# Kernel tuning notes

Measured on AMD Instinct MI355X. Metric: run time of the kernel, lower is better.

## Reference

```python
import jax, jax.numpy as jnp
import numpy as np

HEAD_COUNT = 8  # matches init_kwargs head_count

def _branch(q_in, k_in, v_in, Wq, bq, Wk, bk, Wv, bv):
    # q_in/k_in/v_in: [B, N, D]. Linear (efficient) attention, per-head.
    B, N, D = q_in.shape
    H = HEAD_COUNT
    hd = D // H
    q = q_in @ Wq + bq            # [B, N, D]
    k = k_in @ Wk + bk
    v = v_in @ Wv + bv
    # permute(0,2,1) then contiguous channel slices per head == [B,H,hd,N]
    q = q.reshape(B, N, H, hd).transpose(0, 2, 3, 1)  # [B,H,hd,Nq]
    k = k.reshape(B, N, H, hd).transpose(0, 2, 3, 1)  # [B,H,hd,Nk]
    v = v.reshape(B, N, H, hd).transpose(0, 2, 3, 1)  # [B,H,hd,Nk]
    q = jax.nn.softmax(q, axis=3)  # softmax over sequence positions (torch dim=2)
    k = jax.nn.softmax(k, axis=2)  # softmax over head channels (torch dim=1)
    # context = k @ v^T : [B,H,hd_c,hd_d]
    ctx = jnp.einsum('bhcn,bhdn->bhcd', k, v)
    # attended = context^T @ q : [B,H,hd_d,Nq]
    att = jnp.einsum('bhcd,bhcn->bhdn', ctx, q)
    # concat heads along channel dim, then transpose -> [B, Nq, D]
    return att.reshape(B, D, N).transpose(0, 2, 1)

def setup_inputs() -> dict:
    key = jax.random.key(0)
    ks = jax.random.split(key, 16)
    B, N, D = 4, 8192, 256
    s = 0.02
    inp = {
        'f1': jax.random.normal(ks[0], (B, N, D), jnp.float32),
        'f2': jax.random.normal(ks[1], (B, N, D), jnp.float32),
        'f3': jax.random.normal(ks[2], (B, N, D), jnp.float32),
        'f4': jax.random.normal(ks[3], (B, N, D), jnp.float32),
        'f1_pos_embed': jax.random.normal(ks[4], (B, N, D), jnp.float32),
        'f2_pos_embed': jax.random.normal(ks[5], (B, N, D), jnp.float32),
        'f3_pos_embed': jax.random.normal(ks[6], (B, N, D), jnp.float32),
        'f4_pos_embed': jax.random.normal(ks[7], (B, N, D), jnp.float32),
        'Wq': jax.random.normal(ks[8], (3, D, D), jnp.float32) * s,
        'bq': jax.random.normal(ks[9], (3, D), jnp.float32) * s,
        'Wk': jax.random.normal(ks[10], (3, D, D), jnp.float32) * s,
        'bk': jax.random.normal(ks[11], (3, D), jnp.float32) * s,
        'Wv': jax.random.normal(ks[12], (3, D, D), jnp.float32) * s,
        'bv': jax.random.normal(ks[13], (3, D), jnp.float32) * s,
        'Wrp': jax.random.normal(ks[14], (3 * D, D), jnp.float32) * s,
        'brp': jax.random.normal(ks[15], (D,), jnp.float32) * s,
    }
    return inp

def reference(f1, f2, f3, f4, f1_pos_embed, f2_pos_embed, f3_pos_embed, f4_pos_embed,
              Wq, bq, Wk, bk, Wv, bv, Wrp, brp):
    q_in = f1 + f1_pos_embed
    agg21 = _branch(q_in, f2 + f2_pos_embed, f2, Wq[0], bq[0], Wk[0], bk[0], Wv[0], bv[0])
    agg31 = _branch(q_in, f3 + f3_pos_embed, f3, Wq[1], bq[1], Wk[1], bk[1], Wv[1], bv[1])
    agg41 = _branch(q_in, f4 + f4_pos_embed, f4, Wq[2], bq[2], Wk[2], bk[2], Wv[2], bv[2])
    out = jnp.concatenate([agg21, agg31, agg41], axis=-1)  # [B, N, 3D]
    return out @ Wrp + brp  # dropout p=0.0 -> identity
```

## Files before the change

kernel.cpp:

```cpp
#include <hip/hip_runtime.h>
#include <hip/hip_bf16.h>

typedef __attribute__((ext_vector_type(8))) short short8;
typedef __attribute__((ext_vector_type(4))) float floatx4;
typedef __attribute__((ext_vector_type(16))) float floatx16;

#define N_SEQ 8192
#define M_ROWS 32768

__device__ __forceinline__ unsigned short f2bf(float f) {
    unsigned int x = __builtin_bit_cast(unsigned int, f);
    x += 0x7fff + ((x >> 16) & 1);
    return (unsigned short)(x >> 16);
}

__global__ __launch_bounds__(256) void transpose_w(
    const float* __restrict__ Wq, const float* __restrict__ Wk,
    const float* __restrict__ Wv, unsigned short* __restrict__ Wt)
{
    int job = blockIdx.x;
    int k = blockIdx.y;
    int n = threadIdx.x;
    const float* src =
        (job < 3) ? (Wq + job * 65536) :
        (job < 6) ? (Wk + (job - 3) * 65536) :
                    (Wv + (job - 6) * 65536);
    Wt[(size_t)job * 65536 + n * 256 + k] = f2bf(src[k * 256 + n]);
}

__global__ __launch_bounds__(256) void projq_kernel(
    const float* __restrict__ f1, const float* __restrict__ p1,
    const float* __restrict__ bq, const unsigned short* __restrict__ Wt,
    unsigned short* __restrict__ expQ, float* __restrict__ S)
{
    __shared__ __align__(16) unsigned short As[64][264];
    int m0 = blockIdx.x * 64;
    int b = m0 >> 13;
    int tid = threadIdx.x;
    int lane = tid & 63, wave = tid >> 6;
    int wm = wave >> 1, wn = wave & 1;
    int quad = lane >> 4, l15 = lane & 15;

    {
        int row = tid >> 2, seg = tid & 3;
        const float* fr = f1 + (size_t)(m0 + row) * 256 + seg * 64;
        const float* pr = p1 + (size_t)(m0 + row) * 256 + seg * 64;
        #pragma unroll
        for (int q = 0; q < 8; q++) {
            float4 x0 = *(const float4*)(fr + q * 8);
            float4 x1 = *(const float4*)(fr + q * 8 + 4);
            float4 y0 = *(const float4*)(pr + q * 8);
            float4 y1 = *(const float4*)(pr + q * 8 + 4);
            short8 v;
            v[0] = (short)f2bf(x0.x + y0.x); v[1] = (short)f2bf(x0.y + y0.y);
            v[2] = (short)f2bf(x0.z + y0.z); v[3] = (short)f2bf(x0.w + y0.w);
            v[4] = (short)f2bf(x1.x + y1.x); v[5] = (short)f2bf(x1.y + y1.y);
            v[6] = (short)f2bf(x1.z + y1.z); v[7] = (short)f2bf(x1.w + y1.w);
            *(short8*)&As[row][seg * 64 + q * 8] = v;
        }
    }
    __syncthreads();

    for (int nj = 0; nj < 6; nj++) {
        int j = nj >> 1;
        int n0 = (nj & 1) * 128;
        const unsigned short* Wj = Wt + (size_t)j * 65536;

        floatx4 acc[2][4];
        #pragma unroll
        for (int sm = 0; sm < 2; sm++)
            #pragma unroll
            for (int sn = 0; sn < 4; sn++)
                #pragma unroll
                for (int r = 0; r < 4; r++) acc[sm][sn][r] = 0.0f;

        #pragma unroll
        for (int ks = 0; ks < 8; ks++) {
            short8 af[2], bfr[4];
            #pragma unroll
            for (int sm = 0; sm < 2; sm++)
                af[sm] = *(const short8*)&As[wm * 32 + sm * 16 + l15][ks * 32 + quad * 8];
            #pragma unroll
            for (int sn = 0; sn < 4; sn++) {
                int ncol = n0 + wn * 64 + sn * 16 + l15;
                bfr[sn] = *(const short8*)(Wj + (size_t)ncol * 256 + ks * 32 + quad * 8);
            }
            #pragma unroll
            for (int sm = 0; sm < 2; sm++)
                #pragma unroll
                for (int sn = 0; sn < 4; sn++)
                    acc[sm][sn] = __builtin_amdgcn_mfma_f32_16x16x32_bf16(
                        af[sm], bfr[sn], acc[sm][sn], 0, 0, 0);
        }

        float colsum[4] = {0.f, 0.f, 0.f, 0.f};
        #pragma unroll
        for (int sm = 0; sm < 2; sm++)
            #pragma unroll
            for (int sn = 0; sn < 4; sn++) {
                float bb = bq[j * 256 + n0 + wn * 64 + sn * 16 + l15];
                #pragma unroll
                for (int r = 0; r < 4; r++) {
                    float e = __expf(acc[sm][sn][r] + bb);
                    colsum[sn] += e;
                    int row = m0 + wm * 32 + sm * 16 + quad * 4 + r;
                    int col = j * 256 + n0 + wn * 64 + sn * 16 + l15;
                    expQ[(size_t)row * 768 + col] = f2bf(e);
                }
            }
        #pragma unroll
        for (int sn = 0; sn < 4; sn++) {
            float v = colsum[sn];
            v += __shfl_xor(v, 16, 64);
            v += __shfl_xor(v, 32, 64);
            if (quad == 0)
                atomicAdd(&S[b * 768 + j * 256 + n0 + wn * 64 + sn * 16 + l15], v);
        }
    }
}

__global__ __launch_bounds__(256) void projkv_ctx(
    const float* __restrict__ f2, const float* __restrict__ f3, const float* __restrict__ f4,
    const float* __restrict__ p2, const float* __restrict__ p3, const float* __restrict__ p4,
    const float* __restrict__ bk, const float* __restrict__ bv,
    const unsigned short* __restrict__ Wt, float* __restrict__ ctx)
{
    __shared__ __align__(16) unsigned short Ak[64][264];
    __shared__ __align__(16) unsigned short Av[64][264];

    int blk = blockIdx.x;
    int c = blk & 31;
    int ib = blk >> 5;
    int b = ib & 3, i = ib >> 2;
    const float* fin = ((i == 0) ? f2 : (i == 1) ? f3 : f4) + (size_t)b * N_SEQ * 256;
    const float* pin = ((i == 0) ? p2 : (i == 1) ? p3 : p4) + (size_t)b * N_SEQ * 256;
    const unsigned short* Wk_ = Wt + (size_t)(3 + i) * 65536;
    const unsigned short* Wv_ = Wt + (size_t)(6 + i) * 65536;

    int tid = threadIdx.x;
    int lane = tid & 63, wn = tid >> 6;
    int quad = lane >> 4, l15 = lane & 15;
    int srow = tid >> 2, seg = tid & 3;

    float bkk[4], bvv[4];
    #pragma unroll
    for (int sn = 0; sn < 4; sn++) {
        bkk[sn] = bk[i * 256 + wn * 64 + sn * 16 + l15];
        bvv[sn] = bv[i * 256 + wn * 64 + sn * 16 + l15];
    }

    floatx16 ctxacc[2];
    #pragma unroll
    for (int e = 0; e < 2; e++)
        #pragma unroll
        for (int q = 0; q < 16; q++) ctxacc[e][q] = 0.0f;

    for (int t = 0; t < 4; t++) {
        int m0 = (c + t * 32) * 64;
        __syncthreads();
        {
            const float* fr = fin + (size_t)(m0 + srow) * 256 + seg * 64;
            const float* pr = pin + (size_t)(m0 + srow) * 256 + seg * 64;
            #pragma unroll
            for (int q = 0; q < 8; q++) {
                float4 x0 = *(const float4*)(fr + q * 8);
                float4 x1 = *(const float4*)(fr + q * 8 + 4);
                float4 y0 = *(const float4*)(pr + q * 8);
                float4 y1 = *(const float4*)(pr + q * 8 + 4);
                short8 vv, kk;
                vv[0] = (short)f2bf(x0.x); kk[0] = (short)f2bf(x0.x + y0.x);
                vv[1] = (short)f2bf(x0.y); kk[1] = (short)f2bf(x0.y + y0.y);
                vv[2] = (short)f2bf(x0.z); kk[2] = (short)f2bf(x0.z + y0.z);
                vv[3] = (short)f2bf(x0.w); kk[3] = (short)f2bf(x0.w + y0.w);
                vv[4] = (short)f2bf(x1.x); kk[4] = (short)f2bf(x1.x + y1.x);
                vv[5] = (short)f2bf(x1.y); kk[5] = (short)f2bf(x1.y + y1.y);
                vv[6] = (short)f2bf(x1.z); kk[6] = (short)f2bf(x1.z + y1.z);
                vv[7] = (short)f2bf(x1.w); kk[7] = (short)f2bf(x1.w + y1.w);
                *(short8*)&Av[srow][seg * 64 + q * 8] = vv;
                *(short8*)&Ak[srow][seg * 64 + q * 8] = kk;
            }
        }
        __syncthreads();

        floatx4 acc[4][4];
        #pragma unroll
        for (int sm = 0; sm < 4; sm++)
            #pragma unroll
            for (int sn = 0; sn < 4; sn++)
                #pragma unroll
                for (int r = 0; r < 4; r++) acc[sm][sn][r] = 0.0f;
        #pragma unroll
        for (int ks = 0; ks < 8; ks++) {
            short8 af[4], bfr[4];
            #pragma unroll
            for (int sm = 0; sm < 4; sm++)
                af[sm] = *(const short8*)&Ak[sm * 16 + l15][ks * 32 + quad * 8];
            #pragma unroll
            for (int sn = 0; sn < 4; sn++) {
                int ncol = wn * 64 + sn * 16 + l15;
                bfr[sn] = *(const short8*)(Wk_ + (size_t)ncol * 256 + ks * 32 + quad * 8);
            }
            #pragma unroll
            for (int sm = 0; sm < 4; sm++)
                #pragma unroll
                for (int sn = 0; sn < 4; sn++)
                    acc[sm][sn] = __builtin_amdgcn_mfma_f32_16x16x32_bf16(
                        af[sm], bfr[sn], acc[sm][sn], 0, 0, 0);
        }
        #pragma unroll
        for (int sm = 0; sm < 4; sm++)
            #pragma unroll
            for (int sn = 0; sn < 4; sn++)
                #pragma unroll
                for (int r = 0; r < 4; r++)
                    acc[sm][sn][r] = __expf(acc[sm][sn][r] + bkk[sn]);
        #pragma unroll
        for (int sm = 0; sm < 4; sm++)
            #pragma unroll
            for (int r = 0; r < 4; r++) {
                float t0 = acc[sm][0][r] + acc[sm][1][r];
                t0 += __shfl_xor(t0, 1, 64);
                t0 += __shfl_xor(t0, 2, 64);
                t0 += __shfl_xor(t0, 4, 64);
                t0 += __shfl_xor(t0, 8, 64);
                float i0 = 1.0f / t0;
                acc[sm][0][r] *= i0; acc[sm][1][r] *= i0;
                float t1 = acc[sm][2][r] + acc[sm][3][r];
                t1 += __shfl_xor(t1, 1, 64);
                t1 += __shfl_xor(t1, 2, 64);
                t1 += __shfl_xor(t1, 4, 64);
                t1 += __shfl_xor(t1, 8, 64);
                float i1 = 1.0f / t1;
                acc[sm][2][r] *= i1; acc[sm][3][r] *= i1;
            }
        __syncthreads();
        #pragma unroll
        for (int sm = 0; sm < 4; sm++)
            #pragma unroll
            for (int sn = 0; sn < 4; sn++)
                #pragma unroll
                for (int r = 0; r < 4; r++)
                    Ak[sm * 16 + quad * 4 + r][wn * 64 + sn * 16 + l15] = f2bf(acc[sm][sn][r]);

        #pragma unroll
        for (int sm = 0; sm < 4; sm++)
            #pragma unroll
            for (int sn = 0; sn < 4; sn++)
                #pragma unroll
                for (int r = 0; r < 4; r++) acc[sm][sn][r] = 0.0f;
        #pragma unroll
        for (int ks = 0; ks < 8; ks++) {
            short8 af[4], bfr[4];
            #pragma unroll
            for (int sm = 0; sm < 4; sm++)
                af[sm] = *(const short8*)&Av[sm * 16 + l15][ks * 32 + quad * 8];
            #pragma unroll
            for (int sn = 0; sn < 4; sn++) {
                int ncol = wn * 64 + sn * 16 + l15;
                bfr[sn] = *(const short8*)(Wv_ + (size_t)ncol * 256 + ks * 32 + quad * 8);
            }
            #pragma unroll
            for (int sm = 0; sm < 4; sm++)
                #pragma unroll
                for (int sn = 0; sn < 4; sn++)
                    acc[sm][sn] = __builtin_amdgcn_mfma_f32_16x16x32_bf16(
                        af[sm], bfr[sn], acc[sm][sn], 0, 0, 0);
        }
        __syncthreads();
        #pragma unroll
        for (int sm = 0; sm < 4; sm++)
            #pragma unroll
            for (int sn = 0; sn < 4; sn++)
                #pragma unroll
                for (int r = 0; r < 4; r++)
                    Av[sm * 16 + quad * 4 + r][wn * 64 + sn * 16 + l15] =
                        f2bf(acc[sm][sn][r] + bvv[sn]);
        __syncthreads();

        #pragma unroll
        for (int e = 0; e < 2; e++) {
            int hc = (wn * 2 + e) * 32 + (lane & 31);
            #pragma unroll
            for (int s = 0; s < 4; s++) {
                short8 afr, bfr2;
                #pragma unroll
                for (int jj = 0; jj < 8; jj++) {
                    int n = s * 16 + (lane >> 5) * 8 + jj;
                    afr[jj]  = (short)Ak[n][hc];
                    bfr2[jj] = (short)Av[n][hc];
                }
                ctxacc[e] = __builtin_amdgcn_mfma_f32_32x32x16_bf16(afr, bfr2, ctxacc[e], 0, 0, 0);
            }
        }
    }

    #pragma unroll
    for (int e = 0; e < 2; e++) {
        int h = wn * 2 + e;
        int g = i * 32 + b * 8 + h;
        int d = lane & 31;
        #pragma unroll
        for (int reg = 0; reg < 16; reg++) {
            int cc = (reg & 3) + 8 * (reg >> 2) + 4 * (lane >> 5);
            atomicAdd(&ctx[(size_t)g * 1024 + cc * 32 + d], ctxacc[e][reg]);
        }
    }
}

__global__ __launch_bounds__(256) void wtilde_kernel(
    const float* __restrict__ ctx, const float* __restrict__ S,
    const float* __restrict__ Wrp, unsigned short* __restrict__ Wtld)
{
    __shared__ float cp[1024];
    int g = blockIdx.x;
    int i = g >> 5, b = (g >> 3) & 3, h = g & 7;
    int t = threadIdx.x;
    #pragma unroll
    for (int q = 0; q < 4; q++) {
        int idx = t + q * 256;
        int c = idx >> 5;
        cp[idx] = ctx[(size_t)g * 1024 + idx] / S[b * 768 + i * 256 + h * 32 + c];
    }
    __syncthreads();
    float accv[32];
    #pragma unroll
    for (int c = 0; c < 32; c++) accv[c] = 0.0f;
    for (int d = 0; d < 32; d++) {
        float w = Wrp[(size_t)(i * 256 + h * 32 + d) * 256 + t];
        #pragma unroll
        for (int c = 0; c < 32; c++) accv[c] += cp[c * 32 + d] * w;
    }
    for (int c = 0; c < 32; c++)
        Wtld[((size_t)b * 256 + t) * 768 + i * 256 + h * 32 + c] = f2bf(accv[c]);
}

__global__ __launch_bounds__(256) void out_kernel(
    const unsigned short* __restrict__ expQ, const unsigned short* __restrict__ Wtld,
    const float* __restrict__ brp, float* __restrict__ outp)
{
    __shared__ __align__(16) unsigned short As[128][72];
    int m0 = blockIdx.x * 128;
    int n0 = blockIdx.y * 128;
    int b = m0 >> 13;
    const unsigned short* Wb = Wtld + (size_t)b * 256 * 768;
    int tid = threadIdx.x;
    int lane = tid & 63, wave = tid >> 6;
    int wm = wave >> 1, wn = wave & 1;
    int quad = lane >> 4, l15 = lane & 15;

    floatx4 acc[4][4];
    #pragma unroll
    for (int a = 0; a < 4; a++)
        #pragma unroll
        for (int cc = 0; cc < 4; cc++)
            #pragma unroll
            for (int r = 0; r < 4; r++) acc[a][cc][r] = 0.0f;

    for (int kt = 0; kt < 12; kt++) {
        __syncthreads();
        #pragma unroll
        for (int p = 0; p < 4; p++) {
            int r = (tid >> 3) + p * 32;
            int kc = (tid & 7) * 8;
            size_t ga = (size_t)(m0 + r) * 768 + kt * 64 + kc;
            *(short8*)&As[r][kc] = *(const short8*)(expQ + ga);
        }
        __syncthreads();
        #pragma unroll
        for (int kc = 0; kc < 64; kc += 32) {
            short8 af[4], bfr[4];
            #pragma unroll
            for (int sm = 0; sm < 4; sm++)
                af[sm] = *(const short8*)&As[wm * 64 + sm * 16 + l15][kc + quad * 8];
            #pragma unroll
            for (int sn = 0; sn < 4; sn++) {
                int ncol = n0 + wn * 64 + sn * 16 + l15;
                bfr[sn] = *(const short8*)(Wb + (size_t)ncol * 768 + kt * 64 + kc + quad * 8);
            }
            #pragma unroll
            for (int sm = 0; sm < 4; sm++)
                #pragma unroll
                for (int sn = 0; sn < 4; sn++)
                    acc[sm][sn] = __builtin_amdgcn_mfma_f32_16x16x32_bf16(
                        af[sm], bfr[sn], acc[sm][sn], 0, 0, 0);
        }
    }

    float bb[4];
    #pragma unroll
    for (int sn = 0; sn < 4; sn++) bb[sn] = brp[n0 + wn * 64 + sn * 16 + l15];
    #pragma unroll
    for (int sm = 0; sm < 4; sm++)
        #pragma unroll
        for (int sn = 0; sn < 4; sn++)
            #pragma unroll
            for (int r = 0; r < 4; r++) {
                int row = m0 + wm * 64 + sm * 16 + quad * 4 + r;
                int col = n0 + wn * 64 + sn * 16 + l15;
                outp[(size_t)row * 256 + col] = acc[sm][sn][r] + bb[sn];
            }
}

extern "C" void kernel_launch(void* const* d_in, const int* in_sizes, int n_in,
                              void* d_out, int out_size, void* d_ws, size_t ws_size,
                              hipStream_t stream)
{
    (void)in_sizes; (void)n_in; (void)out_size; (void)ws_size;
    const float* f1  = (const float*)d_in[0];
    const float* f2  = (const float*)d_in[1];
    const float* f3  = (const float*)d_in[2];
    const float* f4  = (const float*)d_in[3];
    const float* p1  = (const float*)d_in[4];
    const float* p2  = (const float*)d_in[5];
    const float* p3  = (const float*)d_in[6];
    const float* p4  = (const float*)d_in[7];
    const float* Wq  = (const float*)d_in[8];
    const float* bq  = (const float*)d_in[9];
    const float* Wk  = (const float*)d_in[10];
    const float* bk  = (const float*)d_in[11];
    const float* Wv  = (const float*)d_in[12];
    const float* bv  = (const float*)d_in[13];
    const float* Wrp = (const float*)d_in[14];
    const float* brp = (const float*)d_in[15];

    char* ws = (char*)d_ws;
    unsigned short* expQ = (unsigned short*)(ws);
    unsigned short* Wt   = (unsigned short*)(ws + 50331648);
    unsigned short* Wtld = (unsigned short*)(ws + 51511296);
    float*          ctx  = (float*)(ws + 53084160);
    float*          S    = (float*)(ws + 53477376);

    hipMemsetAsync(ctx, 0, 393216 + 12288, stream);

    transpose_w<<<dim3(9, 256), 256, 0, stream>>>(Wq, Wk, Wv, Wt);
    projq_kernel<<<dim3(512), 256, 0, stream>>>(f1, p1, bq, Wt, expQ, S);
    projkv_ctx<<<dim3(384), 256, 0, stream>>>(f2, f3, f4, p2, p3, p4, bk, bv, Wt, ctx);
    wtilde_kernel<<<dim3(96), 256, 0, stream>>>(ctx, S, Wrp, Wtld);
    out_kernel<<<dim3(256, 2), 256, 0, stream>>>(expQ, Wtld, brp, (float*)d_out);
}
```

Before: 481.8 us.

## Restructure K/V projection kernel to 512 threads with flattened tile scheduling

The K/V projection plus context kernel now uses 512-thread blocks with eight waves, each owning one head (32 columns), and a grid of 512 blocks that each process three 64-row tiles from a flattened task index. Context is flushed with atomics whenever a block crosses a batch/branch boundary. The softmax and exp are fused into a single pass. Projected K and V are stored transposed in shared memory so the context MFMA operands load as vectors instead of scalar gathers. The goal is better CU load balance and occupancy plus cheaper LDS access, at the cost of more register pressure and extra atomic flushes at tile-group boundaries.

Measured after the change: 429.7 us. 10.8% less time.

```diff
diff --git a/kernel.cpp b/kernel.cpp
--- a/kernel.cpp
+++ b/kernel.cpp
@@ -2,6 +2,7 @@
 #include <hip/hip_bf16.h>
 
 typedef __attribute__((ext_vector_type(8))) short short8;
+typedef __attribute__((ext_vector_type(4))) short shortx4;
 typedef __attribute__((ext_vector_type(4))) float floatx4;
 typedef __attribute__((ext_vector_type(16))) float floatx16;
 
@@ -119,54 +120,66 @@
     }
 }
 
-__global__ __launch_bounds__(256) void projkv_ctx(
+__global__ __launch_bounds__(512, 4) void projkv_ctx(
     const float* __restrict__ f2, const float* __restrict__ f3, const float* __restrict__ f4,
     const float* __restrict__ p2, const float* __restrict__ p3, const float* __restrict__ p4,
     const float* __restrict__ bk, const float* __restrict__ bv,
     const unsigned short* __restrict__ Wt, float* __restrict__ ctx)
 {
-    __shared__ __align__(16) unsigned short Ak[64][264];
-    __shared__ __align__(16) unsigned short Av[64][264];
-
-    int blk = blockIdx.x;
-    int c = blk & 31;
-    int ib = blk >> 5;
-    int b = ib & 3, i = ib >> 2;
-    const float* fin = ((i == 0) ? f2 : (i == 1) ? f3 : f4) + (size_t)b * N_SEQ * 256;
-    const float* pin = ((i == 0) ? p2 : (i == 1) ? p3 : p4) + (size_t)b * N_SEQ * 256;
-    const unsigned short* Wk_ = Wt + (size_t)(3 + i) * 65536;
-    const unsigned short* Wv_ = Wt + (size_t)(6 + i) * 65536;
+    __shared__ __align__(16) unsigned short sh[36864];
 
     int tid = threadIdx.x;
     int lane = tid & 63, wn = tid >> 6;
     int quad = lane >> 4, l15 = lane & 15;
-    int srow = tid >> 2, seg = tid & 3;
-
-    float bkk[4], bvv[4];
-    #pragma unroll
-    for (int sn = 0; sn < 4; sn++) {
-        bkk[sn] = bk[i * 256 + wn * 64 + sn * 16 + l15];
-        bvv[sn] = bv[i * 256 + wn * 64 + sn * 16 + l15];
-    }
-
-    floatx16 ctxacc[2];
-    #pragma unroll
-    for (int e = 0; e < 2; e++)
-        #pragma unroll
-        for (int q = 0; q < 16; q++) ctxacc[e][q] = 0.0f;
-
-    for (int t = 0; t < 4; t++) {
-        int m0 = (c + t * 32) * 64;
+    int srow = tid >> 3, seg = tid & 7;
+
+    int gbase = -1;
+    int cur_ib = -1;
+    const float *fin = nullptr, *pin = nullptr;
+    const unsigned short *Wk_ = nullptr, *Wv_ = nullptr;
+    float bkk[2] = {0.f, 0.f}, bvv[2] = {0.f, 0.f};
+    floatx16 ctxacc;
+
+    for (int j = 0; j < 3; j++) {
+        int tau = blockIdx.x * 3 + j;
+        int ib = tau >> 7;
+        if (ib != cur_ib) {
+            if (gbase >= 0) {
+                int d = lane & 31;
+                #pragma unroll
+                for (int reg = 0; reg < 16; reg++) {
+                    int cc = (reg & 3) + 8 * (reg >> 2) + 4 * (lane >> 5);
+                    atomicAdd(&ctx[(size_t)gbase * 1024 + cc * 32 + d], ctxacc[reg]);
+                }
+            }
+            cur_ib = ib;
+            int b = ib & 3, i = ib >> 2;
+            fin = ((i == 0) ? f2 : (i == 1) ? f3 : f4) + (size_t)b * N_SEQ * 256;
+            pin = ((i == 0) ? p2 : (i == 1) ? p3 : p4) + (size_t)b * N_SEQ * 256;
+            Wk_ = Wt + (size_t)(3 + i) * 65536;
+            Wv_ = Wt + (size_t)(6 + i) * 65536;
+            #pragma unroll
+            for (int sn = 0; sn < 2; sn++) {
+                bkk[sn] = bk[i * 256 + wn * 32 + sn * 16 + l15];
+                bvv[sn] = bv[i * 256 + wn * 32 + sn * 16 + l15];
+            }
+            gbase = i * 32 + b * 8 + wn;
+            #pragma unroll
+            for (int q = 0; q < 16; q++) ctxacc[q] = 0.0f;
+        }
+        int m0 = (tau & 127) * 64;
+
         __syncthreads();
         {
-            const float* fr = fin + (size_t)(m0 + srow) * 256 + seg * 64;
-            const float* pr = pin + (size_t)(m0 + srow) * 256 + seg * 64;
-            #pragma unroll
-            for (int q = 0; q < 8; q++) {
-                float4 x0 = *(const float4*)(fr + q * 8);
-                float4 x1 = *(const float4*)(fr + q * 8 + 4);
-                float4 y0 = *(const float4*)(pr + q * 8);
-                float4 y1 = *(const float4*)(pr + q * 8 + 4);
+            const float* fr = fin + (size_t)(m0 + srow) * 256;
+            const float* pr = pin + (size_t)(m0 + srow) * 256;
+            #pragma unroll
+            for (int q = 0; q < 4; q++) {
+                int c0 = q * 64 + seg * 8;
+                float4 x0 = *(const float4*)(fr + c0);
+                float4 x1 = *(const float4*)(fr + c0 + 4);
+                float4 y0 = *(const float4*)(pr + c0);
+                float4 y1 = *(const float4*)(pr + c0 + 4);
                 short8 vv, kk;
                 vv[0] = (short)f2bf(x0.x); kk[0] = (short)f2bf(x0.x + y0.x);
                 vv[1] = (short)f2bf(x0.y); kk[1] = (short)f2bf(x0.y + y0.y);
@@ -176,93 +189,84 @@
                 vv[5] = (short)f2bf(x1.y); kk[5] = (short)f2bf(x1.y + y1.y);
                 vv[6] = (short)f2bf(x1.z); kk[6] = (short)f2bf(x1.z + y1.z);
                 vv[7] = (short)f2bf(x1.w); kk[7] = (short)f2bf(x1.w + y1.w);
-                *(short8*)&Av[srow][seg * 64 + q * 8] = vv;
-                *(short8*)&Ak[srow][seg * 64 + q * 8] = kk;
-            }
-        }
-        __syncthreads();
-
-        floatx4 acc[4][4];
+                *(short8*)&sh[srow * 264 + c0] = kk;
+                *(short8*)&sh[18432 + srow * 264 + c0] = vv;
+            }
+        }
+        __syncthreads();
+
+        floatx4 acc[4][2];
         #pragma unroll
         for (int sm = 0; sm < 4; sm++)
             #pragma unroll
-            for (int sn = 0; sn < 4; sn++)
+            for (int sn = 0; sn < 2; sn++)
                 #pragma unroll
                 for (int r = 0; r < 4; r++) acc[sm][sn][r] = 0.0f;
         #pragma unroll
         for (int ks = 0; ks < 8; ks++) {
-            short8 af[4], bfr[4];
-            #pragma unroll
-            for (int sm = 0; sm < 4; sm++)
-                af[sm] = *(const short8*)&Ak[sm * 16 + l15][ks * 32 + quad * 8];
-            #pragma unroll
-            for (int sn = 0; sn < 4; sn++) {
-                int ncol = wn * 64 + sn * 16 + l15;
+            short8 af[4], bfr[2];
+            #pragma unroll
+            for (int sm = 0; sm < 4; sm++)
+                af[sm] = *(const short8*)&sh[(sm * 16 + l15) * 264 + ks * 32 + quad * 8];
+            #pragma unroll
+            for (int sn = 0; sn < 2; sn++) {
+                int ncol = wn * 32 + sn * 16 + l15;
                 bfr[sn] = *(const short8*)(Wk_ + (size_t)ncol * 256 + ks * 32 + quad * 8);
             }
             #pragma unroll
             for (int sm = 0; sm < 4; sm++)
                 #pragma unroll
-                for (int sn = 0; sn < 4; sn++)
+                for (int sn = 0; sn < 2; sn++)
                     acc[sm][sn] = __builtin_amdgcn_mfma_f32_16x16x32_bf16(
                         af[sm], bfr[sn], acc[sm][sn], 0, 0, 0);
         }
         #pragma unroll
         for (int sm = 0; sm < 4; sm++)
             #pragma unroll
-            for (int sn = 0; sn < 4; sn++)
-                #pragma unroll
-                for (int r = 0; r < 4; r++)
-                    acc[sm][sn][r] = __expf(acc[sm][sn][r] + bkk[sn]);
+            for (int r = 0; r < 4; r++) {
+                float e0 = __expf(acc[sm][0][r] + bkk[0]);
+                float e1 = __expf(acc[sm][1][r] + bkk[1]);
+                float t = e0 + e1;
+                t += __shfl_xor(t, 1, 64);
+                t += __shfl_xor(t, 2, 64);
+                t += __shfl_xor(t, 4, 64);
+                t += __shfl_xor(t, 8, 64);
+                float inv = 1.0f / t;
+                acc[sm][0][r] = e0 * inv;
+                acc[sm][1][r] = e1 * inv;
+            }
+        __syncthreads();
         #pragma unroll
         for (int sm = 0; sm < 4; sm++)
             #pragma unroll
-            for (int r = 0; r < 4; r++) {
-                float t0 = acc[sm][0][r] + acc[sm][1][r];
-                t0 += __shfl_xor(t0, 1, 64);
-                t0 += __shfl_xor(t0, 2, 64);
-                t0 += __shfl_xor(t0, 4, 64);
-                t0 += __shfl_xor(t0, 8, 64);
-                float i0 = 1.0f / t0;
-                acc[sm][0][r] *= i0; acc[sm][1][r] *= i0;
-                float t1 = acc[sm][2][r] + acc[sm][3][r];
-                t1 += __shfl_xor(t1, 1, 64);
-                t1 += __shfl_xor(t1, 2, 64);
-                t1 += __shfl_xor(t1, 4, 64);
-                t1 += __shfl_xor(t1, 8, 64);
-                float i1 = 1.0f / t1;
-                acc[sm][2][r] *= i1; acc[sm][3][r] *= i1;
-            }
-        __syncthreads();
+            for (int sn = 0; sn < 2; sn++) {
+                shortx4 v;
+                #pragma unroll
+                for (int r = 0; r < 4; r++) v[r] = (short)f2bf(acc[sm][sn][r]);
+                *(shortx4*)&sh[(wn * 32 + sn * 16 + l15) * 72 + sm * 16 + quad * 4] = v;
+            }
+
         #pragma unroll
         for (int sm = 0; sm < 4; sm++)
             #pragma unroll
-            for (int sn = 0; sn < 4; sn++)
-                #pragma unroll
-                for (int r = 0; r < 4; r++)
-                    Ak[sm * 16 + quad * 4 + r][wn * 64 + sn * 16 + l15] = f2bf(acc[sm][sn][r]);
-
-        #pragma unroll
-        for (int sm = 0; sm < 4; sm++)
-            #pragma unroll
-            for (int sn = 0; sn < 4; sn++)
+            for (int sn = 0; sn < 2; sn++)
                 #pragma unroll
                 for (int r = 0; r < 4; r++) acc[sm][sn][r] = 0.0f;
         #pragma unroll
         for (int ks = 0; ks < 8; ks++) {
-            short8 af[4], bfr[4];
-            #pragma unroll
-            for (int sm = 0; sm < 4; sm++)
-                af[sm] = *(const short8*)&Av[sm * 16 + l15][ks * 32 + quad * 8];
-            #pragma unroll
-            for (int sn = 0; sn < 4; sn++) {
-                int ncol = wn * 64 + sn * 16 + l15;
+            short8 af[4], bfr[2];
+            #pragma unroll
+            for (int sm = 0; sm < 4; sm++)
+                af[sm] = *(const short8*)&sh[18432 + (sm * 16 + l15) * 264 + ks * 32 + quad * 8];
+            #pragma unroll
+            for (int sn = 0; sn < 2; sn++) {
+                int ncol = wn * 32 + sn * 16 + l15;
                 bfr[sn] = *(const short8*)(Wv_ + (size_t)ncol * 256 + ks * 32 + quad * 8);
             }
             #pragma unroll
             for (int sm = 0; sm < 4; sm++)
                 #pragma unroll
-                for (int sn = 0; sn < 4; sn++)
+                for (int sn = 0; sn < 2; sn++)
                     acc[sm][sn] = __builtin_amdgcn_mfma_f32_16x16x32_bf16(
                         af[sm], bfr[sn], acc[sm][sn], 0, 0, 0);
         }
@@ -270,39 +274,31 @@
         #pragma unroll
         for (int sm = 0; sm < 4; sm++)
             #pragma unroll
-            for (int sn = 0; sn < 4; sn++)
-                #pragma unroll
-                for (int r = 0; r < 4; r++)
-                    Av[sm * 16 + quad * 4 + r][wn * 64 + sn * 16 + l15] =
-                        f2bf(acc[sm][sn][r] + bvv[sn]);
-        __syncthreads();
-
-        #pragma unroll
-        for (int e = 0; e < 2; e++) {
-            int hc = (wn * 2 + e) * 32 + (lane & 31);
+            for (int sn = 0; sn < 2; sn++) {
+                shortx4 v;
+                #pragma unroll
+                for (int r = 0; r < 4; r++) v[r] = (short)f2bf(acc[sm][sn][r] + bvv[sn]);
+                *(shortx4*)&sh[18432 + (wn * 32 + sn * 16 + l15) * 72 + sm * 16 + quad * 4] = v;
+            }
+
+        {
+            int hc = wn * 32 + (lane & 31);
+            int nb = (lane >> 5) * 8;
             #pragma unroll
             for (int s = 0; s < 4; s++) {
-                short8 afr, bfr2;
-                #pragma unroll
-                for (int jj = 0; jj < 8; jj++) {
-                    int n = s * 16 + (lane >> 5) * 8 + jj;
-                    afr[jj]  = (short)Ak[n][hc];
-                    bfr2[jj] = (short)Av[n][hc];
-                }
-                ctxacc[e] = __builtin_amdgcn_mfma_f32_32x32x16_bf16(afr, bfr2, ctxacc[e], 0, 0, 0);
-            }
-        }
-    }
-
-    #pragma unroll
-    for (int e = 0; e < 2; e++) {
-        int h = wn * 2 + e;
-        int g = i * 32 + b * 8 + h;
+                short8 afr  = *(const short8*)&sh[hc * 72 + s * 16 + nb];
+                short8 bfr2 = *(const short8*)&sh[18432 + hc * 72 + s * 16 + nb];
+                ctxacc = __builtin_amdgcn_mfma_f32_32x32x16_bf16(afr, bfr2, ctxacc, 0, 0, 0);
+            }
+        }
+    }
+
+    if (gbase >= 0) {
         int d = lane & 31;
         #pragma unroll
         for (int reg = 0; reg < 16; reg++) {
             int cc = (reg & 3) + 8 * (reg >> 2) + 4 * (lane >> 5);
-            atomicAdd(&ctx[(size_t)g * 1024 + cc * 32 + d], ctxacc[e][reg]);
+            atomicAdd(&ctx[(size_t)gbase * 1024 + cc * 32 + d], ctxacc[reg]);
         }
     }
 }
@@ -434,7 +430,7 @@
 
     transpose_w<<<dim3(9, 256), 256, 0, stream>>>(Wq, Wk, Wv, Wt);
     projq_kernel<<<dim3(512), 256, 0, stream>>>(f1, p1, bq, Wt, expQ, S);
-    projkv_ctx<<<dim3(384), 256, 0, stream>>>(f2, f3, f4, p2, p3, p4, bk, bv, Wt, ctx);
+    projkv_ctx<<<dim3(512), 512, 0, stream>>>(f2, f3, f4, p2, p3, p4, bk, bv, Wt, ctx);
     wtilde_kernel<<<dim3(96), 256, 0, stream>>>(ctx, S, Wrp, Wtld);
     out_kernel<<<dim3(256, 2), 256, 0, stream>>>(expQ, Wtld, brp, (float*)d_out);
 }
```
